# Kernel optimization log

Hardware: AMD Instinct MI355X
Metric: run time of the kernel (lower is better)

The kernel has to match this reference:

```python
import jax, jax.numpy as jnp
import numpy as np

B, S, D, H = 2, 2048, 2048, 16
HD = D // H  # head_dim = 128


def rotate_half(x):
    x1, x2 = x[..., : x.shape[-1] // 2], x[..., x.shape[-1] // 2 :]
    return jnp.concatenate((-x2, x1), axis=-1)


def setup_inputs() -> dict:
    key = jax.random.key(0)
    ks = jax.random.split(key, 6)
    x = jax.random.normal(ks[0], (B, S, D), dtype=jnp.float32)
    # RoPE cos/sin tables, shape [B, S, head_dim]
    inv_freq = 1.0 / (10000.0 ** (np.arange(0, HD, 2, dtype=np.float32) / HD))
    t = np.arange(S, dtype=np.float32)
    freqs = np.outer(t, inv_freq)                      # [S, HD/2]
    emb = np.concatenate([freqs, freqs], axis=-1)      # [S, HD]
    cos = jnp.broadcast_to(jnp.cos(emb), (B, S, HD)).astype(jnp.float32)
    sin = jnp.broadcast_to(jnp.sin(emb), (B, S, HD)).astype(jnp.float32)
    attn_mask = jnp.zeros((B, S), dtype=jnp.float32)   # additive 2D mask
    scale = 0.02
    wq = jax.random.normal(ks[1], (D, D), dtype=jnp.float32) * scale
    wk = jax.random.normal(ks[2], (D, D), dtype=jnp.float32) * scale
    wv = jax.random.normal(ks[3], (D, D), dtype=jnp.float32) * scale
    wo = jax.random.normal(ks[4], (D, D), dtype=jnp.float32) * scale
    return {"x": x, "cos": cos, "sin": sin, "attn_mask": attn_mask,
            "wq": wq, "wk": wk, "wv": wv, "wo": wo}


def reference(x, cos, sin, attn_mask, wq, wk, wv, wo):
    b, s, d = x.shape
    # fused-style QKV projections (nn.Linear: y = x @ W.T), reshape to [b,h,s,hd]
    def proj(w):
        return jnp.einsum('bsd,ed->bse', x, w).reshape(b, s, H, HD).transpose(0, 2, 1, 3)
    q, k, v = proj(wq), proj(wk), proj(wv)
    # RoPE: cos/sin [b,s,hd] -> broadcast over heads
    c = cos[:, None, :, :]
    sn = sin[:, None, :, :]
    q = q * c + rotate_half(q) * sn
    k = k * c + rotate_half(k) * sn
    # SDPA with additive 2D mask -> [b,1,1,s]
    scores = jnp.einsum('bhqd,bhkd->bhqk', q, k) / jnp.sqrt(jnp.float32(HD))
    scores = scores + attn_mask[:, None, None, :]
    attn = jax.nn.softmax(scores, axis=-1)
    out = jnp.einsum('bhqk,bhkd->bhqd', attn, v)
    out = out.transpose(0, 2, 1, 3).reshape(b, s, d)
    return jnp.einsum('bsd,ed->bse', out, wo)
```

## Files before the change

kernel.cpp:

```cpp
#include <hip/hip_runtime.h>

#define B_  2
#define S_  2048
#define D_  2048
#define H_  16
#define HD_ 128

typedef float  f32x4  __attribute__((ext_vector_type(4)));
typedef __bf16 bf16x8 __attribute__((ext_vector_type(8)));

__device__ __forceinline__ void gl16(const void* g, void* l) {
  __builtin_amdgcn_global_load_lds(
      (const __attribute__((address_space(1))) unsigned int*)g,
      (__attribute__((address_space(3))) unsigned int*)l, 16, 0, 0);
}

__device__ __forceinline__ ushort f2bf(float f) {
  union { float f; unsigned u; } v; v.f = f;
  unsigned r = v.u + 0x7FFFu + ((v.u >> 16) & 1u);
  return (ushort)(r >> 16);
}
__device__ __forceinline__ float bf2f(ushort b) {
  union { unsigned u; float f; } v; v.u = ((unsigned)b) << 16;
  return v.f;
}
__device__ __forceinline__ f32x4 fzero() {
  f32x4 v; v[0] = 0.f; v[1] = 0.f; v[2] = 0.f; v[3] = 0.f; return v;
}

__global__ void cvt4(const float* __restrict__ s, ushort* __restrict__ d, int n4) {
  int i = blockIdx.x * blockDim.x + threadIdx.x;
  if (i >= n4) return;
  float4 v = ((const float4*)s)[i];
  ushort4 o = make_ushort4(f2bf(v.x), f2bf(v.y), f2bf(v.z), f2bf(v.w));
  ((ushort4*)d)[i] = o;
}

template<int MODE>
__global__ __launch_bounds__(256, 2)
void gemm_bt(const ushort* __restrict__ A, const ushort* __restrict__ Bp,
             void* __restrict__ Cp, int M, int N, int K)
{
  __shared__ __align__(16) ushort lds[2][2][128 * 32];
  const int tid  = threadIdx.x;
  const int wave = tid >> 6, lane = tid & 63;
  const int qt = lane >> 4, ln = lane & 15;
  const int wr = wave >> 1, wc = wave & 1;
  const int bm = blockIdx.x * 128, bn = blockIdx.y * 128;

  f32x4 acc[4][4];
#pragma unroll
  for (int a = 0; a < 4; ++a)
#pragma unroll
    for (int b = 0; b < 4; ++b) acc[a][b] = fzero();

  auto stage = [&](int buf, int kt) {
#pragma unroll
    for (int it = 0; it < 2; ++it) {
      int c = it * 256 + tid;
      int row = c >> 2, ch = c & 3;
      int chs = ch ^ ((row >> 1) & 3);
      gl16(A  + (size_t)(bm + row) * K + kt + chs * 8,
           (void*)&lds[buf][0][(it * 256 + wave * 64) * 8]);
      gl16(Bp + (size_t)(bn + row) * K + kt + chs * 8,
           (void*)&lds[buf][1][(it * 256 + wave * 64) * 8]);
    }
  };

  const int nk = K >> 5;
  stage(0, 0);
  int cur = 0;
  for (int kt = 0; kt < nk; ++kt) {
    __syncthreads();
    if (kt + 1 < nk) stage(cur ^ 1, (kt + 1) << 5);
    bf16x8 af[4], bfr[4];
#pragma unroll
    for (int mf = 0; mf < 4; ++mf) {
      int row = wr * 64 + mf * 16 + ln;
      int sl = qt ^ ((row >> 1) & 3);
      af[mf] = *(const bf16x8*)&lds[cur][0][row * 32 + sl * 8];
    }
#pragma unroll
    for (int nf = 0; nf < 4; ++nf) {
      int row = wc * 64 + nf * 16 + ln;
      int sl = qt ^ ((row >> 1) & 3);
      bfr[nf] = *(const bf16x8*)&lds[cur][1][row * 32 + sl * 8];
    }
#pragma unroll
    for (int mf = 0; mf < 4; ++mf)
#pragma unroll
      for (int nf = 0; nf < 4; ++nf)
        acc[mf][nf] = __builtin_amdgcn_mfma_f32_16x16x32_bf16(
            af[mf], bfr[nf], acc[mf][nf], 0, 0, 0);
    cur ^= 1;
  }

#pragma unroll
  for (int mf = 0; mf < 4; ++mf)
#pragma unroll
    for (int nf = 0; nf < 4; ++nf) {
      int m0 = bm + wr * 64 + mf * 16 + qt * 4;
      int n  = bn + wc * 64 + nf * 16 + ln;
#pragma unroll
      for (int i = 0; i < 4; ++i) {
        int m = m0 + i;
        if (MODE == 0) {
          ((float*)Cp)[(size_t)m * N + n] = acc[mf][nf][i];
        } else {
          int b = m >> 11, s = m & 2047;
          int h = n >> 7,  d = n & 127;
          if (MODE == 1)
            ((ushort*)Cp)[(((size_t)b * H_ + h) * S_ + s) * HD_ + d] = f2bf(acc[mf][nf][i]);
          else
            ((ushort*)Cp)[(((size_t)b * H_ + h) * HD_ + d) * S_ + s] = f2bf(acc[mf][nf][i]);
        }
      }
    }
}

__global__ void rope_qk(ushort* __restrict__ Q, ushort* __restrict__ Kt,
                        const float* __restrict__ cs, const float* __restrict__ sn)
{
  int t = blockIdx.x * 256 + threadIdx.x;
  int d  = t & 63;
  int rr = t >> 6;
  int isk = rr >> 16;
  int bhs = rr & 65535;
  int s = bhs & 2047;
  int b = bhs >> 15;
  ushort* P = isk ? Kt : Q;
  size_t ro = (size_t)bhs * HD_;
  float q0 = bf2f(P[ro + d]), q1 = bf2f(P[ro + d + 64]);
  size_t ci = ((size_t)b * S_ + s) * HD_ + d;
  float c0 = cs[ci], s0 = sn[ci], c1 = cs[ci + 64], s1 = sn[ci + 64];
  P[ro + d]      = f2bf(q0 * c0 - q1 * s0);
  P[ro + d + 64] = f2bf(q1 * c1 + q0 * s1);
}

__global__ __launch_bounds__(512, 4)
void flash(const ushort* __restrict__ Q, const ushort* __restrict__ Kk,
           const ushort* __restrict__ VT, const float* __restrict__ mask,
           ushort* __restrict__ O)
{
  __shared__ __align__(16) ushort kt_s[2][64 * 128];
  __shared__ __align__(16) ushort vt_s[2][128 * 64];
  __shared__ __align__(16) ushort pt[8][16 * 64];

  const int tid = threadIdx.x;
  const int wave = tid >> 6, lane = tid & 63;
  const int qt = lane >> 4, ln = lane & 15;
  const int bh = blockIdx.x, b = bh >> 4, h = bh & 15;
  const size_t base  = (size_t)bh * S_ * HD_;
  const size_t baseT = (size_t)bh * HD_ * S_;
  const int q0 = blockIdx.y * 128 + wave * 16;

  bf16x8 qf[4];
  {
    const ushort* qrow = Q + base + (size_t)(q0 + ln) * HD_;
#pragma unroll
    for (int kk = 0; kk < 4; ++kk)
      qf[kk] = *(const bf16x8*)(qrow + kk * 32 + qt * 8);
  }

  f32x4 accO[8];
#pragma unroll
  for (int i = 0; i < 8; ++i) accO[i] = fzero();
  float mrun[4] = {-1e30f, -1e30f, -1e30f, -1e30f};
  float lrun[4] = {0.f, 0.f, 0.f, 0.f};
  const float scale = 0.08838834764831845f;

  auto stageKV = [&](int buf, int k0) {
#pragma unroll
    for (int it = 0; it < 2; ++it) {
      int c = it * 512 + tid;
      int row = c >> 4, ch = c & 15;
      int chs = ch ^ (row & 7);
      gl16(Kk + base + (size_t)(k0 + row) * HD_ + chs * 8,
           (void*)&kt_s[buf][(it * 512 + wave * 64) * 8]);
    }
#pragma unroll
    for (int it = 0; it < 2; ++it) {
      int c = it * 512 + tid;
      int row = c >> 3, ch = c & 7;
      int chs = ch ^ (row & 7);
      gl16(VT + baseT + (size_t)row * S_ + k0 + chs * 8,
           (void*)&vt_s[buf][(it * 512 + wave * 64) * 8]);
    }
  };

  stageKV(0, 0);
  int cur = 0;
  for (int k0 = 0; k0 < S_; k0 += 64) {
    __syncthreads();
    if (k0 + 64 < S_) stageKV(cur ^ 1, k0 + 64);

    f32x4 sc[4];
    __builtin_amdgcn_s_setprio(1);
#pragma unroll
    for (int nf = 0; nf < 4; ++nf) {
      f32x4 a = fzero();
      int row = nf * 16 + ln;
#pragma unroll
      for (int kk = 0; kk < 4; ++kk) {
        int sl = (kk * 4 + qt) ^ (row & 7);
        bf16x8 kf = *(const bf16x8*)&kt_s[cur][row * 128 + sl * 8];
        a = __builtin_amdgcn_mfma_f32_16x16x32_bf16(qf[kk], kf, a, 0, 0, 0);
      }
      sc[nf] = a;
    }
    __builtin_amdgcn_s_setprio(0);

    float sv[4][4];
#pragma unroll
    for (int nf = 0; nf < 4; ++nf) {
      float mk = mask[(size_t)b * S_ + k0 + nf * 16 + ln];
#pragma unroll
      for (int i = 0; i < 4; ++i) sv[nf][i] = sc[nf][i] * scale + mk;
    }
    float fsc[4];
#pragma unroll
    for (int i = 0; i < 4; ++i) {
      float m = fmaxf(fmaxf(sv[0][i], sv[1][i]), fmaxf(sv[2][i], sv[3][i]));
#pragma unroll
      for (int o = 1; o < 16; o <<= 1) m = fmaxf(m, __shfl_xor(m, o));
      float mn = fmaxf(mrun[i], m);
      fsc[i] = __expf(mrun[i] - mn);
      mrun[i] = mn;
    }
#pragma unroll
    for (int i = 0; i < 4; ++i) {
      float t = 0.f;
      int r = qt * 4 + i;
#pragma unroll
      for (int nf = 0; nf < 4; ++nf) {
        float p = __expf(sv[nf][i] - mrun[i]);
        ushort pq = f2bf(p);
        int c = nf * 16 + ln;
        pt[wave][r * 64 + ((c >> 3) ^ (r & 7)) * 8 + (c & 7)] = pq;
        t += bf2f(pq);
      }
#pragma unroll
      for (int o = 1; o < 16; o <<= 1) t += __shfl_xor(t, o);
      lrun[i] = lrun[i] * fsc[i] + t;
    }
#pragma unroll
    for (int nfo = 0; nfo < 8; ++nfo)
#pragma unroll
      for (int i = 0; i < 4; ++i) accO[nfo][i] *= fsc[i];

    __builtin_amdgcn_s_setprio(1);
#pragma unroll
    for (int kk2 = 0; kk2 < 2; ++kk2) {
      int psl = (kk2 * 4 + qt) ^ (ln & 7);
      bf16x8 pf = *(const bf16x8*)&pt[wave][ln * 64 + psl * 8];
#pragma unroll
      for (int nfo = 0; nfo < 8; ++nfo) {
        int vrow = nfo * 16 + ln;
        int vsl = (kk2 * 4 + qt) ^ (vrow & 7);
        bf16x8 vf = *(const bf16x8*)&vt_s[cur][vrow * 64 + vsl * 8];
        accO[nfo] = __builtin_amdgcn_mfma_f32_16x16x32_bf16(pf, vf, accO[nfo], 0, 0, 0);
      }
    }
    __builtin_amdgcn_s_setprio(0);
    cur ^= 1;
  }

  float inv[4];
#pragma unroll
  for (int i = 0; i < 4; ++i) inv[i] = 1.f / lrun[i];
#pragma unroll
  for (int nfo = 0; nfo < 8; ++nfo)
#pragma unroll
    for (int i = 0; i < 4; ++i) {
      size_t idx = ((size_t)b * S_ + q0 + qt * 4 + i) * D_ + h * HD_ + nfo * 16 + ln;
      O[idx] = f2bf(accO[nfo][i] * inv[i]);
    }
}

extern "C" void kernel_launch(void* const* d_in, const int* in_sizes, int n_in,
                              void* d_out, int out_size, void* d_ws, size_t ws_size,
                              hipStream_t stream)
{
  if (n_in != 8) return;
  if (in_sizes[0] != 8388608) return;
  if (in_sizes[3] != 4096)    return;
  if (out_size != 8388608) return;
  if (ws_size < (size_t)96 * 1024 * 1024) return;

  const float* x    = (const float*)d_in[0];
  const float* cosb = (const float*)d_in[1];
  const float* sinb = (const float*)d_in[2];
  const float* mask = (const float*)d_in[3];
  const float* wq   = (const float*)d_in[4];
  const float* wk   = (const float*)d_in[5];
  const float* wv   = (const float*)d_in[6];
  const float* wo   = (const float*)d_in[7];

  char* ws = (char*)d_ws;
  ushort* xb  = (ushort*)(ws);
  ushort* wqb = (ushort*)(ws + 16777216);
  ushort* wkb = (ushort*)(ws + 25165824);
  ushort* wvb = (ushort*)(ws + 33554432);
  ushort* wob = (ushort*)(ws + 41943040);
  ushort* Qb  = (ushort*)(ws + 50331648);
  ushort* Kb  = (ushort*)(ws + 67108864);
  ushort* VTb = (ushort*)(ws + 83886080);
  ushort* AOb = xb;

  cvt4<<<8192, 256, 0, stream>>>(x,  xb,  2097152);
  cvt4<<<4096, 256, 0, stream>>>(wq, wqb, 1048576);
  cvt4<<<4096, 256, 0, stream>>>(wk, wkb, 1048576);
  cvt4<<<4096, 256, 0, stream>>>(wv, wvb, 1048576);
  cvt4<<<4096, 256, 0, stream>>>(wo, wob, 1048576);

  dim3 gg(32, 16);
  gemm_bt<1><<<gg, 256, 0, stream>>>(xb, wqb, Qb,  4096, 2048, 2048);
  gemm_bt<1><<<gg, 256, 0, stream>>>(xb, wkb, Kb,  4096, 2048, 2048);
  gemm_bt<3><<<gg, 256, 0, stream>>>(xb, wvb, VTb, 4096, 2048, 2048);

  rope_qk<<<32768, 256, 0, stream>>>(Qb, Kb, cosb, sinb);

  flash<<<dim3(32, 16), 512, 0, stream>>>(Qb, Kb, VTb, mask, AOb);

  gemm_bt<0><<<gg, 256, 0, stream>>>(AOb, wob, d_out, 4096, 2048, 2048);
}
```

Baseline: 338.6 us.

## Use exp2 softmax with lazy rescaling and deferred row-sum reduction in flash kernel

New measurement: 318.0 us. -6.1%, faster.

```diff
diff --git a/kernel.cpp b/kernel.cpp
--- a/kernel.cpp
+++ b/kernel.cpp
@@ -26,6 +26,9 @@
 }
 __device__ __forceinline__ f32x4 fzero() {
   f32x4 v; v[0] = 0.f; v[1] = 0.f; v[2] = 0.f; v[3] = 0.f; return v;
+}
+__device__ __forceinline__ float exp2x(float x) {
+  return __builtin_amdgcn_exp2f(x);
 }
 
 __global__ void cvt4(const float* __restrict__ s, ushort* __restrict__ d, int n4) {
@@ -153,6 +156,7 @@
   const size_t base  = (size_t)bh * S_ * HD_;
   const size_t baseT = (size_t)bh * HD_ * S_;
   const int q0 = blockIdx.y * 128 + wave * 16;
+  const float L2E = 1.4426950408889634f;
 
   bf16x8 qf[4];
   {
@@ -167,7 +171,7 @@
   for (int i = 0; i < 8; ++i) accO[i] = fzero();
   float mrun[4] = {-1e30f, -1e30f, -1e30f, -1e30f};
   float lrun[4] = {0.f, 0.f, 0.f, 0.f};
-  const float scale = 0.08838834764831845f;
+  const float scale2 = 0.08838834764831845f * L2E;
 
   auto stageKV = [&](int buf, int k0) {
 #pragma unroll
@@ -213,19 +217,30 @@
     float sv[4][4];
 #pragma unroll
     for (int nf = 0; nf < 4; ++nf) {
-      float mk = mask[(size_t)b * S_ + k0 + nf * 16 + ln];
-#pragma unroll
-      for (int i = 0; i < 4; ++i) sv[nf][i] = sc[nf][i] * scale + mk;
-    }
-    float fsc[4];
+      float mk = mask[(size_t)b * S_ + k0 + nf * 16 + ln] * L2E;
+#pragma unroll
+      for (int i = 0; i < 4; ++i) sv[nf][i] = sc[nf][i] * scale2 + mk;
+    }
+    float pmax[4];
 #pragma unroll
     for (int i = 0; i < 4; ++i) {
       float m = fmaxf(fmaxf(sv[0][i], sv[1][i]), fmaxf(sv[2][i], sv[3][i]));
 #pragma unroll
       for (int o = 1; o < 16; o <<= 1) m = fmaxf(m, __shfl_xor(m, o));
-      float mn = fmaxf(mrun[i], m);
-      fsc[i] = __expf(mrun[i] - mn);
-      mrun[i] = mn;
+      pmax[i] = m;
+    }
+    bool need = (pmax[0] > mrun[0] + 8.f) | (pmax[1] > mrun[1] + 8.f) |
+                (pmax[2] > mrun[2] + 8.f) | (pmax[3] > mrun[3] + 8.f);
+    if (__any(need)) {
+#pragma unroll
+      for (int i = 0; i < 4; ++i) {
+        float mn = fmaxf(mrun[i], pmax[i]);
+        float fsc = exp2x(mrun[i] - mn);
+        mrun[i] = mn;
+        lrun[i] *= fsc;
+#pragma unroll
+        for (int nfo = 0; nfo < 8; ++nfo) accO[nfo][i] *= fsc;
+      }
     }
 #pragma unroll
     for (int i = 0; i < 4; ++i) {
@@ -233,20 +248,14 @@
       int r = qt * 4 + i;
 #pragma unroll
       for (int nf = 0; nf < 4; ++nf) {
-        float p = __expf(sv[nf][i] - mrun[i]);
-        ushort pq = f2bf(p);
+        float p = exp2x(sv[nf][i] - mrun[i]);
+        __bf16 pb = (__bf16)p;
         int c = nf * 16 + ln;
-        pt[wave][r * 64 + ((c >> 3) ^ (r & 7)) * 8 + (c & 7)] = pq;
-        t += bf2f(pq);
-      }
-#pragma unroll
-      for (int o = 1; o < 16; o <<= 1) t += __shfl_xor(t, o);
-      lrun[i] = lrun[i] * fsc[i] + t;
-    }
-#pragma unroll
-    for (int nfo = 0; nfo < 8; ++nfo)
-#pragma unroll
-      for (int i = 0; i < 4; ++i) accO[nfo][i] *= fsc[i];
+        *(__bf16*)&pt[wave][r * 64 + ((c >> 3) ^ (r & 7)) * 8 + (c & 7)] = pb;
+        t += (float)pb;
+      }
+      lrun[i] += t;
+    }
 
     __builtin_amdgcn_s_setprio(1);
 #pragma unroll
@@ -267,7 +276,12 @@
 
   float inv[4];
 #pragma unroll
-  for (int i = 0; i < 4; ++i) inv[i] = 1.f / lrun[i];
+  for (int i = 0; i < 4; ++i) {
+    float t = lrun[i];
+#pragma unroll
+    for (int o = 1; o < 16; o <<= 1) t += __shfl_xor(t, o);
+    inv[i] = 1.f / t;
+  }
 #pragma unroll
   for (int nfo = 0; nfo < 8; ++nfo)
 #pragma unroll
```

## Transpose QK^T MFMA layout, use exp2 softmax with lazy rescaling

Applied to the files above, without the earlier changes.

After: 304.3 us. 10.1% less time.

```diff
diff --git a/kernel.cpp b/kernel.cpp
--- a/kernel.cpp
+++ b/kernel.cpp
@@ -8,6 +8,7 @@
 
 typedef float  f32x4  __attribute__((ext_vector_type(4)));
 typedef __bf16 bf16x8 __attribute__((ext_vector_type(8)));
+typedef __bf16 bf16x4 __attribute__((ext_vector_type(4)));
 
 __device__ __forceinline__ void gl16(const void* g, void* l) {
   __builtin_amdgcn_global_load_lds(
@@ -26,6 +27,9 @@
 }
 __device__ __forceinline__ f32x4 fzero() {
   f32x4 v; v[0] = 0.f; v[1] = 0.f; v[2] = 0.f; v[3] = 0.f; return v;
+}
+__device__ __forceinline__ float exp2x(float x) {
+  return __builtin_amdgcn_exp2f(x);
 }
 
 __global__ void cvt4(const float* __restrict__ s, ushort* __restrict__ d, int n4) {
@@ -153,6 +157,7 @@
   const size_t base  = (size_t)bh * S_ * HD_;
   const size_t baseT = (size_t)bh * HD_ * S_;
   const int q0 = blockIdx.y * 128 + wave * 16;
+  const float L2E = 1.4426950408889634f;
 
   bf16x8 qf[4];
   {
@@ -165,9 +170,9 @@
   f32x4 accO[8];
 #pragma unroll
   for (int i = 0; i < 8; ++i) accO[i] = fzero();
-  float mrun[4] = {-1e30f, -1e30f, -1e30f, -1e30f};
-  float lrun[4] = {0.f, 0.f, 0.f, 0.f};
-  const float scale = 0.08838834764831845f;
+  float mrun = -1e30f;
+  float lrun = 0.f;
+  const float scale2 = 0.08838834764831845f * L2E;
 
   auto stageKV = [&](int buf, int k0) {
 #pragma unroll
@@ -204,7 +209,7 @@
       for (int kk = 0; kk < 4; ++kk) {
         int sl = (kk * 4 + qt) ^ (row & 7);
         bf16x8 kf = *(const bf16x8*)&kt_s[cur][row * 128 + sl * 8];
-        a = __builtin_amdgcn_mfma_f32_16x16x32_bf16(qf[kk], kf, a, 0, 0, 0);
+        a = __builtin_amdgcn_mfma_f32_16x16x32_bf16(kf, qf[kk], a, 0, 0, 0);
       }
       sc[nf] = a;
     }
@@ -213,46 +218,54 @@
     float sv[4][4];
 #pragma unroll
     for (int nf = 0; nf < 4; ++nf) {
-      float mk = mask[(size_t)b * S_ + k0 + nf * 16 + ln];
-#pragma unroll
-      for (int i = 0; i < 4; ++i) sv[nf][i] = sc[nf][i] * scale + mk;
-    }
-    float fsc[4];
-#pragma unroll
-    for (int i = 0; i < 4; ++i) {
-      float m = fmaxf(fmaxf(sv[0][i], sv[1][i]), fmaxf(sv[2][i], sv[3][i]));
-#pragma unroll
-      for (int o = 1; o < 16; o <<= 1) m = fmaxf(m, __shfl_xor(m, o));
-      float mn = fmaxf(mrun[i], m);
-      fsc[i] = __expf(mrun[i] - mn);
-      mrun[i] = mn;
-    }
-#pragma unroll
-    for (int i = 0; i < 4; ++i) {
-      float t = 0.f;
-      int r = qt * 4 + i;
-#pragma unroll
-      for (int nf = 0; nf < 4; ++nf) {
-        float p = __expf(sv[nf][i] - mrun[i]);
-        ushort pq = f2bf(p);
-        int c = nf * 16 + ln;
-        pt[wave][r * 64 + ((c >> 3) ^ (r & 7)) * 8 + (c & 7)] = pq;
-        t += bf2f(pq);
-      }
-#pragma unroll
-      for (int o = 1; o < 16; o <<= 1) t += __shfl_xor(t, o);
-      lrun[i] = lrun[i] * fsc[i] + t;
-    }
-#pragma unroll
-    for (int nfo = 0; nfo < 8; ++nfo)
-#pragma unroll
-      for (int i = 0; i < 4; ++i) accO[nfo][i] *= fsc[i];
+      float4 mk = *(const float4*)&mask[(size_t)b * S_ + k0 + nf * 16 + qt * 4];
+      sv[nf][0] = sc[nf][0] * scale2 + mk.x * L2E;
+      sv[nf][1] = sc[nf][1] * scale2 + mk.y * L2E;
+      sv[nf][2] = sc[nf][2] * scale2 + mk.z * L2E;
+      sv[nf][3] = sc[nf][3] * scale2 + mk.w * L2E;
+    }
+
+    float m = sv[0][0];
+#pragma unroll
+    for (int nf = 0; nf < 4; ++nf)
+#pragma unroll
+      for (int i = 0; i < 4; ++i) m = fmaxf(m, sv[nf][i]);
+    m = fmaxf(m, __shfl_xor(m, 16));
+    m = fmaxf(m, __shfl_xor(m, 32));
+
+    if (__any(m > mrun + 8.f)) {
+      float mn = fmaxf(mrun, m);
+      float fsc = exp2x(mrun - mn);
+      mrun = mn;
+      lrun *= fsc;
+#pragma unroll
+      for (int i = 0; i < 4; ++i) {
+        float fq = __shfl(fsc, qt * 4 + i);
+#pragma unroll
+        for (int nfo = 0; nfo < 8; ++nfo) accO[nfo][i] *= fq;
+      }
+    }
+
+    float t = 0.f;
+#pragma unroll
+    for (int nf = 0; nf < 4; ++nf) {
+      bf16x4 p4;
+#pragma unroll
+      for (int i = 0; i < 4; ++i) {
+        float p = exp2x(sv[nf][i] - mrun);
+        p4[i] = (__bf16)p;
+        t += (float)p4[i];
+      }
+      int g = (nf * 2 + (qt >> 1)) ^ (ln & 7);
+      *(bf16x4*)&pt[wave][ln * 64 + g * 8 + (qt & 1) * 4] = p4;
+    }
+    lrun += t;
 
     __builtin_amdgcn_s_setprio(1);
 #pragma unroll
     for (int kk2 = 0; kk2 < 2; ++kk2) {
-      int psl = (kk2 * 4 + qt) ^ (ln & 7);
-      bf16x8 pf = *(const bf16x8*)&pt[wave][ln * 64 + psl * 8];
+      int gr = (kk2 * 4 + qt) ^ (ln & 7);
+      bf16x8 pf = *(const bf16x8*)&pt[wave][ln * 64 + gr * 8];
 #pragma unroll
       for (int nfo = 0; nfo < 8; ++nfo) {
         int vrow = nfo * 16 + ln;
@@ -265,9 +278,12 @@
     cur ^= 1;
   }
 
+  lrun += __shfl_xor(lrun, 16);
+  lrun += __shfl_xor(lrun, 32);
+  float inv_own = 1.f / lrun;
   float inv[4];
 #pragma unroll
-  for (int i = 0; i < 4; ++i) inv[i] = 1.f / lrun[i];
+  for (int i = 0; i < 4; ++i) inv[i] = __shfl(inv_own, qt * 4 + i);
 #pragma unroll
   for (int nfo = 0; nfo < 8; ++nfo)
 #pragma unroll
```
